# Kernel tuning notes

Measured on AMD Instinct MI355X. Metric: run time of the kernel, lower is better.

## Reference

```python
import jax, jax.numpy as jnp
import numpy as np

B, N, DIM = 2, 4096, 512
HEADS, HEAD_DIM = 8, 64
INNER = HEADS * HEAD_DIM


def setup_inputs() -> dict:
    key = jax.random.key(0)
    k1, k2, k3 = jax.random.split(key, 3)
    x = jax.random.normal(k1, (B, N, DIM), dtype=jnp.float32)
    w_qkv = jax.random.normal(k2, (DIM, 3 * INNER), dtype=jnp.float32) * (DIM ** -0.5)
    temperature = jnp.asarray(np.log(HEAD_DIM ** -0.5), dtype=jnp.float32)
    w_out = jax.random.normal(k3, (INNER, DIM), dtype=jnp.float32) * (INNER ** -0.5)
    b_out = jnp.zeros((DIM,), dtype=jnp.float32)
    return {"x": x, "w_qkv": w_qkv, "temperature": temperature, "w_out": w_out, "b_out": b_out}


def reference(x, w_qkv, temperature, w_out, b_out):
    b, n, _ = x.shape
    qkv = x @ w_qkv                                   # (B, N, 3*inner)
    q, k, v = jnp.split(qkv, 3, axis=-1)
    # Faithful to original: raw reshape (NOT transpose) into (B, H, N, d)
    q = q.reshape(b, HEADS, n, HEAD_DIM)
    k = k.reshape(b, HEADS, n, HEAD_DIM)
    v = v.reshape(b, HEADS, n, HEAD_DIM)
    scores = jnp.einsum('bhnd,bhmd->bhnm', q, k) * jnp.exp(temperature)
    mask = jnp.eye(n, dtype=bool)                     # diagonal self-mask
    mask_value = jnp.finfo(scores.dtype).min
    scores = jnp.where(mask, mask_value, scores)
    attn = jax.nn.softmax(scores, axis=-1)
    out = jnp.einsum('bhnm,bhmd->bhnd', attn, v)      # (B, H, N, d)
    # Faithful to original: raw reshape (NOT transpose) back to (B, N, H*d)
    out = out.reshape(b, n, HEADS * HEAD_DIM)
    return out @ w_out + b_out                        # dropout inactive at inference
```

## Files before the change

kernel.cpp:

```cpp
#include <hip/hip_runtime.h>


typedef __bf16 bf16;
typedef __bf16 bf16x8 __attribute__((ext_vector_type(8)));
typedef __bf16 bf16x4 __attribute__((ext_vector_type(4)));
typedef float  f32x4  __attribute__((ext_vector_type(4)));

#define MFMA_BF16(a, b, c) __builtin_amdgcn_mfma_f32_16x16x32_bf16((a), (b), (c), 0, 0, 0)

__device__ __forceinline__ void gld_lds16(void* lds, const void* g) {
  __builtin_amdgcn_global_load_lds(
      (const __attribute__((address_space(1))) void*)g,
      (__attribute__((address_space(3))) void*)lds, 16, 0, 0);
}


__global__ void cast4_kernel(const float* __restrict__ in, bf16* __restrict__ out, int n4) {
  int i = blockIdx.x * 256 + threadIdx.x;
  if (i >= n4) return;
  float4 v = ((const float4*)in)[i];
  bf16x4 o;
  o[0] = (bf16)v.x; o[1] = (bf16)v.y; o[2] = (bf16)v.z; o[3] = (bf16)v.w;
  *(bf16x4*)(out + 4 * i) = o;
}

__global__ void wtrans_kernel(const float* __restrict__ in, bf16* __restrict__ out, int C) {
  __shared__ float tile[64 * 65];
  const int t = threadIdx.x;
  const int c0 = blockIdx.x * 64, r0 = blockIdx.y * 64;
#pragma unroll
  for (int p = 0; p < 16; p++) {
    int idx = p * 256 + t, r = idx >> 6, c = idx & 63;
    tile[r * 65 + c] = in[(r0 + r) * C + c0 + c];
  }
  __syncthreads();
#pragma unroll
  for (int p = 0; p < 16; p++) {
    int idx = p * 256 + t, c = idx >> 6, r = idx & 63;
    out[(size_t)(c0 + c) * 512 + r0 + r] = (bf16)tile[r * 65 + c];
  }
}

__global__ void vtrans_kernel(const bf16* __restrict__ V, bf16* __restrict__ Vt) {
  __shared__ bf16 tile[64 * 65];
  const int t = threadIdx.x;
  const size_t base = (size_t)blockIdx.y << 18;
  const int n0 = blockIdx.x * 64;
#pragma unroll
  for (int p = 0; p < 16; p++) {
    int idx = p * 256 + t, r = idx >> 6, c = idx & 63;
    tile[r * 65 + c] = V[base + (size_t)(n0 + r) * 64 + c];
  }
  __syncthreads();
#pragma unroll
  for (int p = 0; p < 16; p++) {
    int idx = p * 256 + t, d = idx >> 6, n = idx & 63;
    Vt[base + (size_t)d * 4096 + n0 + n] = tile[n * 65 + d];
  }
}


template<int EPI, int WNT>
__global__ __launch_bounds__(256) void gemm_bt(
    const bf16* __restrict__ A, const bf16* __restrict__ Bt,
    bf16* __restrict__ oQ, bf16* __restrict__ oK, bf16* __restrict__ oV,
    float* __restrict__ oC, const float* __restrict__ bias,
    const float* __restrict__ temp)
{
  __shared__ bf16 As[128 * 32];
  __shared__ bf16 Bs[WNT * 32 * 32];

  const int t    = threadIdx.x;
  const int lane = t & 63;
  const int w    = t >> 6;
  const int mm   = lane & 15;
  const int q    = lane >> 4;
  const int wm   = w >> 1, wn = w & 1;
  const int m0   = blockIdx.y * 128;
  const int n0   = blockIdx.x * (WNT * 32);

  const int srow = t >> 2, sch = t & 3;
  const int gch  = sch ^ ((srow >> 1) & 3);
  const bf16* Ab = A  + (m0 + srow) * 512 + gch * 8;
  const bf16* Bb = Bt + (n0 + srow) * 512 + gch * 8;
  bf16* Asl = As + t * 8;
  bf16* Bsl = Bs + t * 8;

  const int fslot = (q ^ ((mm >> 1) & 3)) * 8;

  const f32x4 zero4 = {0.f, 0.f, 0.f, 0.f};
  f32x4 acc[4][WNT];
#pragma unroll
  for (int i = 0; i < 4; i++)
#pragma unroll
    for (int j = 0; j < WNT; j++) acc[i][j] = zero4;

  for (int k0 = 0; k0 < 512; k0 += 32) {
    __syncthreads();
    gld_lds16(Asl,        Ab + k0);
    gld_lds16(Asl + 2048, Ab + 64 * 512 + k0);
    gld_lds16(Bsl,        Bb + k0);
    if (WNT == 4) gld_lds16(Bsl + 2048, Bb + 64 * 512 + k0);
    __syncthreads();

    bf16x8 af[4], bfv[WNT];
#pragma unroll
    for (int i = 0; i < 4; i++)
      af[i] = *(const bf16x8*)(As + (wm * 64 + i * 16 + mm) * 32 + fslot);
#pragma unroll
    for (int j = 0; j < WNT; j++)
      bfv[j] = *(const bf16x8*)(Bs + (wn * (WNT * 16) + j * 16 + mm) * 32 + fslot);

#pragma unroll
    for (int i = 0; i < 4; i++)
#pragma unroll
      for (int j = 0; j < WNT; j++)
        acc[i][j] = MFMA_BF16(af[i], bfv[j], acc[i][j]);
  }

  if (EPI == 0) {
    const float scale = __expf(temp[0]) * 1.44269504088896f;
#pragma unroll
    for (int i = 0; i < 4; i++) {
      const int row = m0 + wm * 64 + i * 16 + q * 4;
#pragma unroll
      for (int j = 0; j < WNT; j++) {
        const int col = n0 + wn * (WNT * 16) + j * 16 + mm;
        bf16* dst; int c2; float s;
        if (col < 512)       { dst = oQ; c2 = col;        s = scale; }
        else if (col < 1024) { dst = oK; c2 = col - 512;  s = 1.0f;  }
        else                 { dst = oV; c2 = col - 1024; s = 1.0f;  }
#pragma unroll
        for (int r = 0; r < 4; r++)
          dst[(size_t)(row + r) * 512 + c2] = (bf16)(acc[i][j][r] * s);
      }
    }
  } else {
#pragma unroll
    for (int i = 0; i < 4; i++) {
      const int row = m0 + wm * 64 + i * 16 + q * 4;
#pragma unroll
      for (int j = 0; j < WNT; j++) {
        const int col = n0 + wn * (WNT * 16) + j * 16 + mm;
        const float b = bias[col];
#pragma unroll
        for (int r = 0; r < 4; r++)
          oC[(size_t)(row + r) * 512 + col] = acc[i][j][r] + b;
      }
    }
  }
}


template<int SPLIT>
__global__ __launch_bounds__(256, 3) void attn_kernel(
    const bf16* __restrict__ Q, const bf16* __restrict__ Kb,
    const bf16* __restrict__ Vt, bf16* __restrict__ O,
    float* __restrict__ Opart, float* __restrict__ Lpart)
{
  __shared__ bf16 Ks[64 * 64];
  __shared__ bf16 Vs[64 * 64];
  __shared__ bf16 Ps[4 * 64 * 72];

  const int t    = threadIdx.x;
  const int lane = t & 63;
  const int w    = t >> 6;
  const int mm   = lane & 15;
  const int q    = lane >> 4;
  const int bh   = blockIdx.y;
  const int q0   = blockIdx.x * 256;
  const int z    = blockIdx.z;
  const size_t hb = (size_t)bh << 18;
  const bf16* Qh = Q  + hb;
  const bf16* Kh = Kb + hb;
  const bf16* Vh = Vt + hb;
  const int q0w  = q0 + w * 64;

  int tlo, tn;
  if (SPLIT == 1)      { tlo = 0;                               tn = 64; }
  else if (SPLIT == 2) { tlo = z * 32;                          tn = 32; }
  else                 { tlo = (z == 0) ? 0 : (z == 1 ? 22 : 43); tn = (z == 0) ? 22 : 21; }

  bf16x8 qf[4][2];
#pragma unroll
  for (int i = 0; i < 4; i++)
#pragma unroll
    for (int ks = 0; ks < 2; ks++)
      qf[i][ks] = *(const bf16x8*)(Qh + (size_t)(q0w + i * 16 + mm) * 64 + ks * 32 + q * 8);

  const f32x4 zero4 = {0.f, 0.f, 0.f, 0.f};
  f32x4 o[4][4];
  f32x4 lacc[4];
#pragma unroll
  for (int i = 0; i < 4; i++) {
    lacc[i] = zero4;
#pragma unroll
    for (int dj = 0; dj < 4; dj++) o[i][dj] = zero4;
  }

  bf16x8 onesf;
#pragma unroll
  for (int e = 0; e < 8; e++) onesf[e] = (bf16)1.0f;

  const int r0 = t >> 3, c0 = t & 7;
  const int g0 = c0 ^ (r0 & 7);
  bf16* Ksl = Ks + t * 8;
  bf16* Vsl = Vs + t * 8;
  bf16* pw  = Ps + w * (64 * 72);

  for (int it = 0; it < tn; it++) {
    const int kv0 = (tlo + it) * 64;
    __syncthreads();
    gld_lds16(Ksl,        Kh + (size_t)(kv0 + r0) * 64 + g0 * 8);
    gld_lds16(Ksl + 2048, Kh + (size_t)(kv0 + 32 + r0) * 64 + g0 * 8);
    gld_lds16(Vsl,        Vh + (size_t)r0 * 4096 + kv0 + g0 * 8);
    gld_lds16(Vsl + 2048, Vh + (size_t)(32 + r0) * 4096 + kv0 + g0 * 8);
    __syncthreads();

    const bool diag = (kv0 == q0w);

#pragma unroll
    for (int jm = 0; jm < 4; jm++) {
      const int krow = jm * 16 + mm;
      const int sw = krow & 7;
      bf16x8 kf0 = *(const bf16x8*)(Ks + krow * 64 + ((q)     ^ sw) * 8);
      bf16x8 kf1 = *(const bf16x8*)(Ks + krow * 64 + ((4 + q) ^ sw) * 8);
#pragma unroll
      for (int i = 0; i < 4; i++) {
        f32x4 zacc = MFMA_BF16(kf0, qf[i][0], zero4);
        f32x4 sv   = MFMA_BF16(kf1, qf[i][1], zacc);
        if (diag && jm == i && (mm >> 2) == q) sv[mm & 3] = -1e30f;
        bf16x4 pk;
#pragma unroll
        for (int r = 0; r < 4; r++)
          pk[r] = (bf16)__builtin_amdgcn_exp2f(sv[r]);
        *(bf16x4*)(pw + (i * 16 + mm) * 72 + jm * 16 + q * 4) = pk;
      }
    }
    __asm__ volatile("s_waitcnt lgkmcnt(0)" ::: "memory");

#pragma unroll
    for (int ks = 0; ks < 2; ks++) {
      bf16x8 vf[4];
#pragma unroll
      for (int dj = 0; dj < 4; dj++) {
        const int d = dj * 16 + mm;
        vf[dj] = *(const bf16x8*)(Vs + d * 64 + ((ks * 4 + q) ^ (d & 7)) * 8);
      }
#pragma unroll
      for (int i = 0; i < 4; i++) {
        bf16x8 pf = *(const bf16x8*)(pw + (i * 16 + mm) * 72 + ks * 32 + q * 8);
#pragma unroll
        for (int dj = 0; dj < 4; dj++)
          o[i][dj] = MFMA_BF16(pf, vf[dj], o[i][dj]);
        lacc[i] = MFMA_BF16(pf, onesf, lacc[i]);
      }
    }
  }

  if (SPLIT == 1) {
    bf16* Oh = O + hb;
#pragma unroll
    for (int i = 0; i < 4; i++) {
      const int rowb = q0w + i * 16 + q * 4;
#pragma unroll
      for (int r = 0; r < 4; r++) {
        const float rinv = 1.0f / lacc[i][r];
#pragma unroll
        for (int dj = 0; dj < 4; dj++)
          Oh[(size_t)(rowb + r) * 64 + dj * 16 + mm] = (bf16)(o[i][dj][r] * rinv);
      }
    }
  } else {
    float* Op = Opart + ((size_t)z << 22) + hb;
    float* Lp = Lpart + (z << 16) + (bh << 12);
#pragma unroll
    for (int i = 0; i < 4; i++) {
      const int rowb = q0w + i * 16 + q * 4;
      if (mm == 0) {
#pragma unroll
        for (int r = 0; r < 4; r++) Lp[rowb + r] = lacc[i][r];
      }
#pragma unroll
      for (int dj = 0; dj < 4; dj++)
#pragma unroll
        for (int r = 0; r < 4; r++)
          Op[(size_t)(rowb + r) * 64 + dj * 16 + mm] = o[i][dj][r];
    }
  }
}

template<int SPLIT>
__global__ void merge_kernel(const float* __restrict__ Op, const float* __restrict__ Lp,
                             bf16* __restrict__ Ob) {
  const int g = blockIdx.x * 256 + threadIdx.x;
  const int f = g * 4;
  const int row = f >> 6;
  float l = 0.f;
  float4 a = {0.f, 0.f, 0.f, 0.f};
#pragma unroll
  for (int zz = 0; zz < SPLIT; zz++) {
    l += Lp[(zz << 16) + row];
    const float4 b = *(const float4*)(Op + ((size_t)zz << 22) + f);
    a.x += b.x; a.y += b.y; a.z += b.z; a.w += b.w;
  }
  const float rinv = 1.0f / l;
  bf16x4 o;
  o[0] = (bf16)(a.x * rinv);
  o[1] = (bf16)(a.y * rinv);
  o[2] = (bf16)(a.z * rinv);
  o[3] = (bf16)(a.w * rinv);
  *(bf16x4*)(Ob + f) = o;
}


extern "C" void kernel_launch(void* const* d_in, const int* in_sizes, int n_in,
                              void* d_out, int out_size, void* d_ws, size_t ws_size,
                              hipStream_t stream) {
  const float* x      = (const float*)d_in[0];
  const float* w_qkv  = (const float*)d_in[1];
  const float* temp   = (const float*)d_in[2];
  const float* w_out  = (const float*)d_in[3];
  const float* b_out  = (const float*)d_in[4];
  float* out          = (float*)d_out;

  char* ws = (char*)d_ws;
  bf16*  Xb    = (bf16*)(ws);
  bf16*  Wt    = (bf16*)(ws + (size_t)(8u  << 20));
  bf16*  Qb    = (bf16*)(ws + (size_t)(10u << 20));
  bf16*  Kb    = (bf16*)(ws + (size_t)(18u << 20));
  bf16*  Vb    = (bf16*)(ws + (size_t)(26u << 20));
  bf16*  Vtb   = (bf16*)(ws + (size_t)(34u << 20));
  bf16*  Ob    = (bf16*)(ws + (size_t)(42u << 20));
  bf16*  Wot   = (bf16*)(ws + (size_t)(50u << 20));
  float* Lpart = (float*)(ws + (size_t)(51u << 20));
  float* Opart = (float*)(ws + (size_t)(52u << 20));

  const int split = (ws_size >= ((size_t)103u << 20)) ? 3
                  : (ws_size >= ((size_t)86u  << 20)) ? 2 : 1;

  cast4_kernel<<<4096, 256, 0, stream>>>(x, Xb, (8192 * 512) / 4);
  wtrans_kernel<<<dim3(24, 8), 256, 0, stream>>>(w_qkv, Wt, 1536);
  wtrans_kernel<<<dim3(8, 8), 256, 0, stream>>>(w_out, Wot, 512);

  gemm_bt<0, 4><<<dim3(12, 64), 256, 0, stream>>>(Xb, Wt, Qb, Kb, Vb, nullptr, nullptr, temp);

  vtrans_kernel<<<dim3(64, 16), 256, 0, stream>>>(Vb, Vtb);

  if (split == 3) {
    attn_kernel<3><<<dim3(16, 16, 3), 256, 0, stream>>>(Qb, Kb, Vtb, nullptr, Opart, Lpart);
    merge_kernel<3><<<4096, 256, 0, stream>>>(Opart, Lpart, Ob);
  } else if (split == 2) {
    attn_kernel<2><<<dim3(16, 16, 2), 256, 0, stream>>>(Qb, Kb, Vtb, nullptr, Opart, Lpart);
    merge_kernel<2><<<4096, 256, 0, stream>>>(Opart, Lpart, Ob);
  } else {
    attn_kernel<1><<<dim3(16, 16, 1), 256, 0, stream>>>(Qb, Kb, Vtb, Ob, nullptr, nullptr);
  }

  gemm_bt<1, 2><<<dim3(8, 64), 256, 0, stream>>>(Ob, Wot, nullptr, nullptr, nullptr, out, b_out, nullptr);
}
```

Baseline: 207.5 us.

## Double-buffer K/V tiles in attention with 32-wide KV tiles and swizzled P

The attention kernel now works on 32-key KV tiles held in two LDS buffers, so the loads for the next tile are issued before computing the current one. This drops the second barrier per iteration and overlaps global-to-LDS loads with MFMA work. The P buffer shrinks to a 32-wide, XOR-swizzled layout to avoid bank conflicts, and the split-2 path is removed. In exchange the loop runs twice as many iterations, each with less work, and the diagonal-mask check is now computed per subtile.

```diff
diff --git a/kernel.cpp b/kernel.cpp
--- a/kernel.cpp
+++ b/kernel.cpp
@@ -158,9 +158,9 @@
     const bf16* __restrict__ Vt, bf16* __restrict__ O,
     float* __restrict__ Opart, float* __restrict__ Lpart)
 {
-  __shared__ bf16 Ks[64 * 64];
-  __shared__ bf16 Vs[64 * 64];
-  __shared__ bf16 Ps[4 * 64 * 72];
+  __shared__ bf16 Ks[2][32 * 64];
+  __shared__ bf16 Vs[2][64 * 32];
+  __shared__ bf16 Ps[4][64 * 32];
 
   const int t    = threadIdx.x;
   const int lane = t & 63;
@@ -177,9 +177,8 @@
   const int q0w  = q0 + w * 64;
 
   int tlo, tn;
-  if (SPLIT == 1)      { tlo = 0;                               tn = 64; }
-  else if (SPLIT == 2) { tlo = z * 32;                          tn = 32; }
-  else                 { tlo = (z == 0) ? 0 : (z == 1 ? 22 : 43); tn = (z == 0) ? 22 : 21; }
+  if (SPLIT == 1)      { tlo = 0;                              tn = 128; }
+  else                 { tlo = (z == 0) ? 0 : (z == 1 ? 43 : 86); tn = (z == 2) ? 42 : 43; }
 
   bf16x8 qf[4][2];
 #pragma unroll
@@ -202,59 +201,68 @@
 #pragma unroll
   for (int e = 0; e < 8; e++) onesf[e] = (bf16)1.0f;
 
-  const int r0 = t >> 3, c0 = t & 7;
-  const int g0 = c0 ^ (r0 & 7);
-  bf16* Ksl = Ks + t * 8;
-  bf16* Vsl = Vs + t * 8;
-  bf16* pw  = Ps + w * (64 * 72);
+  const int skv = t >> 3, sc8 = t & 7;
+  const int gK  = sc8 ^ (skv & 7);
+  const int sd  = t >> 2, sc4 = t & 3;
+  const int gV  = sc4 ^ ((sd >> 2) & 3);
+  const bf16* KgB = Kh + (size_t)skv * 64 + gK * 8;
+  const bf16* VgB = Vh + (size_t)sd * 4096 + gV * 8;
+  bf16* pw = &Ps[w][0];
+
+  {
+    const int kv0 = tlo * 32;
+    gld_lds16(&Ks[0][t * 8], KgB + (size_t)kv0 * 64);
+    gld_lds16(&Vs[0][t * 8], VgB + kv0);
+  }
 
   for (int it = 0; it < tn; it++) {
-    const int kv0 = (tlo + it) * 64;
+    const int buf = it & 1;
     __syncthreads();
-    gld_lds16(Ksl,        Kh + (size_t)(kv0 + r0) * 64 + g0 * 8);
-    gld_lds16(Ksl + 2048, Kh + (size_t)(kv0 + 32 + r0) * 64 + g0 * 8);
-    gld_lds16(Vsl,        Vh + (size_t)r0 * 4096 + kv0 + g0 * 8);
-    gld_lds16(Vsl + 2048, Vh + (size_t)(32 + r0) * 4096 + kv0 + g0 * 8);
-    __syncthreads();
-
-    const bool diag = (kv0 == q0w);
-
-#pragma unroll
-    for (int jm = 0; jm < 4; jm++) {
+    if (it + 1 < tn) {
+      const int kvn = (tlo + it + 1) * 32;
+      gld_lds16(&Ks[buf ^ 1][t * 8], KgB + (size_t)kvn * 64);
+      gld_lds16(&Vs[buf ^ 1][t * 8], VgB + kvn);
+    }
+
+    const int kv0 = (tlo + it) * 32;
+    const bf16* ks = &Ks[buf][0];
+    const bf16* vs = &Vs[buf][0];
+
+#pragma unroll
+    for (int jm = 0; jm < 2; jm++) {
       const int krow = jm * 16 + mm;
       const int sw = krow & 7;
-      bf16x8 kf0 = *(const bf16x8*)(Ks + krow * 64 + ((q)     ^ sw) * 8);
-      bf16x8 kf1 = *(const bf16x8*)(Ks + krow * 64 + ((4 + q) ^ sw) * 8);
+      bf16x8 kf0 = *(const bf16x8*)(ks + krow * 64 + ((q)     ^ sw) * 8);
+      bf16x8 kf1 = *(const bf16x8*)(ks + krow * 64 + ((4 + q) ^ sw) * 8);
 #pragma unroll
       for (int i = 0; i < 4; i++) {
         f32x4 zacc = MFMA_BF16(kf0, qf[i][0], zero4);
         f32x4 sv   = MFMA_BF16(kf1, qf[i][1], zacc);
-        if (diag && jm == i && (mm >> 2) == q) sv[mm & 3] = -1e30f;
+        if ((q0w + i * 16) == (kv0 + jm * 16) && (mm >> 2) == q)
+          sv[mm & 3] = -1e30f;
         bf16x4 pk;
 #pragma unroll
         for (int r = 0; r < 4; r++)
           pk[r] = (bf16)__builtin_amdgcn_exp2f(sv[r]);
-        *(bf16x4*)(pw + (i * 16 + mm) * 72 + jm * 16 + q * 4) = pk;
+        *(bf16x4*)(pw + (i * 16 + mm) * 32 +
+                   (((jm * 2 + (q >> 1)) ^ (mm & 3)) * 8) + (q & 1) * 4) = pk;
       }
     }
     __asm__ volatile("s_waitcnt lgkmcnt(0)" ::: "memory");
 
-#pragma unroll
-    for (int ks = 0; ks < 2; ks++) {
-      bf16x8 vf[4];
-#pragma unroll
-      for (int dj = 0; dj < 4; dj++) {
-        const int d = dj * 16 + mm;
-        vf[dj] = *(const bf16x8*)(Vs + d * 64 + ((ks * 4 + q) ^ (d & 7)) * 8);
-      }
-#pragma unroll
-      for (int i = 0; i < 4; i++) {
-        bf16x8 pf = *(const bf16x8*)(pw + (i * 16 + mm) * 72 + ks * 32 + q * 8);
-#pragma unroll
-        for (int dj = 0; dj < 4; dj++)
-          o[i][dj] = MFMA_BF16(pf, vf[dj], o[i][dj]);
-        lacc[i] = MFMA_BF16(pf, onesf, lacc[i]);
-      }
+    bf16x8 vf[4];
+#pragma unroll
+    for (int dj = 0; dj < 4; dj++) {
+      const int d = dj * 16 + mm;
+      vf[dj] = *(const bf16x8*)(vs + d * 32 + ((q ^ ((d >> 2) & 3)) * 8));
+    }
+#pragma unroll
+    for (int i = 0; i < 4; i++) {
+      bf16x8 pf = *(const bf16x8*)(pw + (i * 16 + mm) * 32 + ((q ^ (mm & 3)) * 8));
+#pragma unroll
+      for (int dj = 0; dj < 4; dj++)
+        o[i][dj] = MFMA_BF16(pf, vf[dj], o[i][dj]);
+      lacc[i] = MFMA_BF16(pf, onesf, lacc[i]);
     }
   }
 
@@ -336,8 +344,7 @@
   float* Lpart = (float*)(ws + (size_t)(51u << 20));
   float* Opart = (float*)(ws + (size_t)(52u << 20));
 
-  const int split = (ws_size >= ((size_t)103u << 20)) ? 3
-                  : (ws_size >= ((size_t)86u  << 20)) ? 2 : 1;
+  const int split = (ws_size >= ((size_t)103u << 20)) ? 3 : 1;
 
   cast4_kernel<<<4096, 256, 0, stream>>>(x, Xb, (8192 * 512) / 4);
   wtrans_kernel<<<dim3(24, 8), 256, 0, stream>>>(w_qkv, Wt, 1536);
@@ -350,9 +357,6 @@
   if (split == 3) {
     attn_kernel<3><<<dim3(16, 16, 3), 256, 0, stream>>>(Qb, Kb, Vtb, nullptr, Opart, Lpart);
     merge_kernel<3><<<4096, 256, 0, stream>>>(Opart, Lpart, Ob);
-  } else if (split == 2) {
-    attn_kernel<2><<<dim3(16, 16, 2), 256, 0, stream>>>(Qb, Kb, Vtb, nullptr, Opart, Lpart);
-    merge_kernel<2><<<4096, 256, 0, stream>>>(Opart, Lpart, Ob);
   } else {
     attn_kernel<1><<<dim3(16, 16, 1), 256, 0, stream>>>(Qb, Kb, Vtb, Ob, nullptr, nullptr);
   }
```

Measured after the change: 215.2 us. 1.04x slower.
